# Optimization experiments

Hardware: AMD Instinct MI355X
Metric: run time of the kernel (lower is better)

The kernel has to match this reference:

```python
import jax, jax.numpy as jnp
import numpy as np

BUCKET_BINS = jnp.array([0, 1, 2, 3, 4, 5, 7, 8, 9, 10, 15, 16, 31, 32, 63, 64], dtype=jnp.int64)
POS_NUM = 28  # ZHPosTaging.pos_num; table size pos_num + 1


def setup_inputs() -> dict:
    key = jax.random.key(0)
    k1, k2, k3, k4, k5 = jax.random.split(key, 5)
    B, S, D = 4, 2048, 768
    N = 4096
    W, P = 20, 20
    x = jax.random.normal(k1, (B, S, D), dtype=jnp.float32)
    spans = jnp.sort(jax.random.randint(k2, (N, 2), 0, S, dtype=jnp.int64), axis=-1)
    pt_labels = jax.random.randint(k3, (S,), 0, POS_NUM + 1, dtype=jnp.int64)
    width_table = jax.random.normal(k4, (16, W), dtype=jnp.float32)
    pos_table = jax.random.normal(k5, (POS_NUM + 1, P), dtype=jnp.float32)
    return {"x": x, "spans": spans, "pt_labels": pt_labels,
            "width_table": width_table, "pos_table": pos_table}


def reference(x, spans, pt_labels, width_table, pos_table):
    # x: [B,S,D], spans: [N,2] with s0<=s1, pt_labels: [S]
    s0, s1 = spans[:, 0], spans[:, 1]                      # [N]
    width = s1 - s0 + 1                                    # [N], >= 1
    # bucket index: last ix with width >= BUCKET_BINS[ix]
    em = jnp.searchsorted(BUCKET_BINS, width, side='right') - 1
    width_emb = width_table[em]                            # [N,W]
    pos_emb0 = pos_table[pt_labels[s0]]                    # [N,P]
    pos_emb1 = pos_table[pt_labels[s1]]                    # [N,P]
    # segment mean over x[:, s0:s1+1] via exclusive cumsum
    cs = jnp.concatenate([jnp.zeros_like(x[:, :1]), jnp.cumsum(x, axis=1)], axis=1)  # [B,S+1,D]
    span_sum = cs[:, s1 + 1] - cs[:, s0]                   # [B,N,D]
    mean_vec = span_sum / width[None, :, None].astype(x.dtype)
    xs0 = x[:, s0]                                         # [B,N,D]
    xs1 = x[:, s1]                                         # [B,N,D]
    B, N = x.shape[0], spans.shape[0]
    bcast = lambda e: jnp.broadcast_to(e[None], (B, N, e.shape[-1]))
    return jnp.concatenate(
        [mean_vec, xs0, bcast(pos_emb0), xs1, bcast(pos_emb1), bcast(width_emb)],
        axis=-1)                                           # [B,N,3D+2P+W]
```

## Files before the change

### kernel.cpp

```cpp
#include <hip/hip_runtime.h>

#define BB   4
#define SS   2048
#define DD   768
#define NN   4096
#define PW   20
#define CH   16
#define NCH  128
#define ROW  2364
#define DQ   192

typedef float f4 __attribute__((ext_vector_type(4)));

__global__ __launch_bounds__(256) void partial_kernel(const float* __restrict__ x,
                                                      float* __restrict__ partial) {
    int tid = blockIdx.x * 256 + threadIdx.x;
    int b = tid / (NCH * DQ);
    int r = tid - b * (NCH * DQ);
    int c = r / DQ;
    int q = r - c * DQ;
    const f4* xp = (const f4*)x + ((size_t)(b * SS + c * CH)) * DQ + q;
    f4 s = {0.f, 0.f, 0.f, 0.f};
#pragma unroll
    for (int i = 0; i < CH; ++i) s += xp[(size_t)i * DQ];
    ((f4*)partial)[((size_t)(b * NCH + c)) * DQ + q] = s;
}

__global__ __launch_bounds__(256) void prefix_kernel(float* __restrict__ partial) {
    int t = blockIdx.x * 256 + threadIdx.x;
    int b = t / DD;
    int d = t - b * DD;
    float* p = partial + (size_t)b * NCH * DD + d;
    float v[NCH];
#pragma unroll
    for (int c = 0; c < NCH; ++c) v[c] = p[(size_t)c * DD];
    float run = 0.f;
#pragma unroll
    for (int c = 0; c < NCH; ++c) { float nv = run + v[c]; p[(size_t)c * DD] = run; run = nv; }
}

__global__ __launch_bounds__(256) void cumsum_kernel(const float* __restrict__ x,
                                                     const float* __restrict__ partial,
                                                     float* __restrict__ cs) {
    int tid = blockIdx.x * 256 + threadIdx.x;
    int b = tid / (NCH * DQ);
    int r = tid - b * (NCH * DQ);
    int c = r / DQ;
    int q = r - c * DQ;
    f4 run = ((const f4*)partial)[((size_t)(b * NCH + c)) * DQ + q];
    const f4* xp = (const f4*)x + ((size_t)(b * SS + c * CH)) * DQ + q;
    f4*       cp = (f4*)cs + ((size_t)(b * (SS + 1) + c * CH + 1)) * DQ + q;
    if (c == 0) {
        f4 z = {0.f, 0.f, 0.f, 0.f};
        ((f4*)cs)[((size_t)(b * (SS + 1))) * DQ + q] = z;
    }
    f4 v[CH];
#pragma unroll
    for (int i = 0; i < CH; ++i) v[i] = xp[(size_t)i * DQ];
#pragma unroll
    for (int i = 0; i < CH; ++i) { run += v[i]; cp[(size_t)i * DQ] = run; }
}

__global__ __launch_bounds__(192) void gather_kernel(const float* __restrict__ x,
                                                     const int* __restrict__ spans,
                                                     const int* __restrict__ pt_labels,
                                                     const float* __restrict__ wtab,
                                                     const float* __restrict__ ptab,
                                                     const float* __restrict__ cs,
                                                     float* __restrict__ out) {
    int n = blockIdx.x;
    int t = threadIdx.x;

    int s0 = spans[2 * n];
    int s1 = spans[2 * n + 1];
    int width = s1 - s0 + 1;
    float inv_w = 1.0f / (float)width;

    const int bins[15] = {1, 2, 3, 4, 5, 7, 8, 9, 10, 15, 16, 31, 32, 63, 64};
    int em = 0;
#pragma unroll
    for (int i = 0; i < 15; ++i) em += (width >= bins[i]) ? 1 : 0;

    f4 a[BB], c0[BB], v0[BB], v1[BB];
#pragma unroll
    for (int b = 0; b < BB; ++b) {
        const f4* cs0 = (const f4*)cs + ((size_t)(b * (SS + 1) + s0)) * DQ;
        const f4* cs1 = (const f4*)cs + ((size_t)(b * (SS + 1) + s1 + 1)) * DQ;
        const f4* x0  = (const f4*)x  + ((size_t)(b * SS + s0)) * DQ;
        const f4* x1  = (const f4*)x  + ((size_t)(b * SS + s1)) * DQ;
        a[b]  = cs1[t];
        c0[b] = cs0[t];
        v0[b] = x0[t];
        v1[b] = x1[t];
    }
#pragma unroll
    for (int b = 0; b < BB; ++b) {
        f4* o = (f4*)(out + ((size_t)(b * NN) + n) * ROW);
        f4 m = (a[b] - c0[b]) * inv_w;
        __builtin_nontemporal_store(m,     o + t);
        __builtin_nontemporal_store(v0[b], o + 192 + t);
        __builtin_nontemporal_store(v1[b], o + 389 + t);
    }

    if (t < 15) {
        f4 e;
        int slot;
        if (t < 5) {
            int l0 = pt_labels[s0];
            e = ((const f4*)(ptab + l0 * PW))[t];
            slot = 384 + t;
        } else if (t < 10) {
            int l1 = pt_labels[s1];
            e = ((const f4*)(ptab + l1 * PW))[t - 5];
            slot = 581 + (t - 5);
        } else {
            e = ((const f4*)(wtab + em * PW))[t - 10];
            slot = 586 + (t - 10);
        }
#pragma unroll
        for (int b = 0; b < BB; ++b) {
            f4* o = (f4*)(out + ((size_t)(b * NN) + n) * ROW);
            __builtin_nontemporal_store(e, o + slot);
        }
    }
}

extern "C" void kernel_launch(void* const* d_in, const int* in_sizes, int n_in,
                              void* d_out, int out_size, void* d_ws, size_t ws_size,
                              hipStream_t stream) {
    const float* x     = (const float*)d_in[0];
    const int*   spans = (const int*)d_in[1];
    const int*   pt    = (const int*)d_in[2];
    const float* wtab  = (const float*)d_in[3];
    const float* ptab  = (const float*)d_in[4];
    float* out = (float*)d_out;

    float* cs      = (float*)d_ws;
    float* partial = cs + (size_t)BB * (SS + 1) * DD;

    const int NB = (BB * NCH * DQ) / 256;
    partial_kernel<<<NB, 256, 0, stream>>>(x, partial);
    prefix_kernel<<<12, 256, 0, stream>>>(partial);
    cumsum_kernel<<<NB, 256, 0, stream>>>(x, partial, cs);
    gather_kernel<<<NN, 192, 0, stream>>>(x, spans, pt, wtab, ptab, cs, out);
}
```

Measured before the change: 218.9 us.

## Split gather kernel across batch in grid, chunk prefix scan registers

Result: faster. 211.1 us (-3.5%).

```diff
diff --git a/kernel.cpp b/kernel.cpp
--- a/kernel.cpp
+++ b/kernel.cpp
@@ -31,12 +31,19 @@
     int b = t / DD;
     int d = t - b * DD;
     float* p = partial + (size_t)b * NCH * DD + d;
-    float v[NCH];
-#pragma unroll
-    for (int c = 0; c < NCH; ++c) v[c] = p[(size_t)c * DD];
     float run = 0.f;
 #pragma unroll
-    for (int c = 0; c < NCH; ++c) { float nv = run + v[c]; p[(size_t)c * DD] = run; run = nv; }
+    for (int blk = 0; blk < NCH / 32; ++blk) {
+        float v[32];
+#pragma unroll
+        for (int c = 0; c < 32; ++c) v[c] = p[(size_t)(blk * 32 + c) * DD];
+#pragma unroll
+        for (int c = 0; c < 32; ++c) {
+            float nv = run + v[c];
+            p[(size_t)(blk * 32 + c) * DD] = run;
+            run = nv;
+        }
+    }
 }
 
 __global__ __launch_bounds__(256) void cumsum_kernel(const float* __restrict__ x,
@@ -61,7 +68,7 @@
     for (int i = 0; i < CH; ++i) { run += v[i]; cp[(size_t)i * DQ] = run; }
 }
 
-__global__ __launch_bounds__(192) void gather_kernel(const float* __restrict__ x,
+__global__ __launch_bounds__(256) void gather_kernel(const float* __restrict__ x,
                                                      const int* __restrict__ spans,
                                                      const int* __restrict__ pt_labels,
                                                      const float* __restrict__ wtab,
@@ -69,6 +76,7 @@
                                                      const float* __restrict__ cs,
                                                      float* __restrict__ out) {
     int n = blockIdx.x;
+    int b = blockIdx.y;
     int t = threadIdx.x;
 
     int s0 = spans[2 * n];
@@ -81,46 +89,31 @@
 #pragma unroll
     for (int i = 0; i < 15; ++i) em += (width >= bins[i]) ? 1 : 0;
 
-    f4 a[BB], c0[BB], v0[BB], v1[BB];
-#pragma unroll
-    for (int b = 0; b < BB; ++b) {
-        const f4* cs0 = (const f4*)cs + ((size_t)(b * (SS + 1) + s0)) * DQ;
-        const f4* cs1 = (const f4*)cs + ((size_t)(b * (SS + 1) + s1 + 1)) * DQ;
-        const f4* x0  = (const f4*)x  + ((size_t)(b * SS + s0)) * DQ;
-        const f4* x1  = (const f4*)x  + ((size_t)(b * SS + s1)) * DQ;
-        a[b]  = cs1[t];
-        c0[b] = cs0[t];
-        v0[b] = x0[t];
-        v1[b] = x1[t];
-    }
-#pragma unroll
-    for (int b = 0; b < BB; ++b) {
-        f4* o = (f4*)(out + ((size_t)(b * NN) + n) * ROW);
-        f4 m = (a[b] - c0[b]) * inv_w;
-        __builtin_nontemporal_store(m,     o + t);
-        __builtin_nontemporal_store(v0[b], o + 192 + t);
-        __builtin_nontemporal_store(v1[b], o + 389 + t);
-    }
+    const f4* cs0 = (const f4*)cs + ((size_t)(b * (SS + 1) + s0)) * DQ;
+    const f4* cs1 = (const f4*)cs + ((size_t)(b * (SS + 1) + s1 + 1)) * DQ;
+    const f4* x0  = (const f4*)x  + ((size_t)(b * SS + s0)) * DQ;
+    const f4* x1  = (const f4*)x  + ((size_t)(b * SS + s1)) * DQ;
+    f4* o = (f4*)(out + ((size_t)(b * NN) + n) * ROW);
 
-    if (t < 15) {
-        f4 e;
-        int slot;
-        if (t < 5) {
+    if (t < 192) {
+        f4 a  = cs1[t];
+        f4 c0 = cs0[t];
+        f4 v0 = x0[t];
+        f4 v1 = x1[t];
+        f4 m = (a - c0) * inv_w;
+        o[t]       = m;
+        o[192 + t] = v0;
+        o[389 + t] = v1;
+    } else {
+        int u = t - 192;
+        if (u < 5) {
             int l0 = pt_labels[s0];
-            e = ((const f4*)(ptab + l0 * PW))[t];
-            slot = 384 + t;
-        } else if (t < 10) {
+            o[384 + u] = ((const f4*)(ptab + l0 * PW))[u];
+        } else if (u < 10) {
             int l1 = pt_labels[s1];
-            e = ((const f4*)(ptab + l1 * PW))[t - 5];
-            slot = 581 + (t - 5);
-        } else {
-            e = ((const f4*)(wtab + em * PW))[t - 10];
-            slot = 586 + (t - 10);
-        }
-#pragma unroll
-        for (int b = 0; b < BB; ++b) {
-            f4* o = (f4*)(out + ((size_t)(b * NN) + n) * ROW);
-            __builtin_nontemporal_store(e, o + slot);
+            o[581 + (u - 5)] = ((const f4*)(ptab + l1 * PW))[u - 5];
+        } else if (u < 15) {
+            o[586 + (u - 10)] = ((const f4*)(wtab + em * PW))[u - 10];
         }
     }
 }
@@ -142,5 +135,5 @@
     partial_kernel<<<NB, 256, 0, stream>>>(x, partial);
     prefix_kernel<<<12, 256, 0, stream>>>(partial);
     cumsum_kernel<<<NB, 256, 0, stream>>>(x, partial, cs);
-    gather_kernel<<<NN, 192, 0, stream>>>(x, spans, pt, wtab, ptab, cs, out);
+    gather_kernel<<<dim3(NN, BB), 256, 0, stream>>>(x, spans, pt, wtab, ptab, cs, out);
 }
```
